# Kernel tuning notes

Measured on AMD Instinct MI355X. Metric: run time of the kernel, lower is better.

Reference implementation:

```python
import jax, jax.numpy as jnp
import numpy as np

B = 32; NPG = 500; N = B * NPG; E = 256000; F = 1024; OD = 128
DD = 80; TD = 32; NH = 4; DH = TD // NH; DFF = 128; NL = 2
LSUB = 128; MAXLEN = 4 * LSUB
NEG = -1e9; SLOPE = 0.01; EPS = 1e-5


def setup_inputs() -> dict:
    key = jax.random.key(0)
    ks = iter(jax.random.split(key, 64))
    nrm = lambda *s: jax.random.normal(next(ks), s, jnp.float32)
    w = lambda *s: nrm(*s) * 0.02
    inp = {}
    inp["pro1_x"] = nrm(N, F)
    inp["pro2_x"] = nrm(N, F)
    inp["pro1_edge_index"] = jax.random.randint(next(ks), (2, E), 0, N)
    inp["pro2_edge_index"] = jax.random.randint(next(ks), (2, E), 0, N)
    inp["pro1_batch"] = jnp.repeat(jnp.arange(B), NPG)
    inp["pro2_batch"] = jnp.repeat(jnp.arange(B), NPG)
    for nm in ("mas1_straight", "mas1_flipped", "mas2_straight", "mas2_flipped"):
        inp[nm] = nrm(B, LSUB, DD)
        inp[nm + "_lengths"] = jax.random.randint(next(ks), (B,), 1, LSUB + 1)
    inp["gcn1_w"] = w(F, F); inp["gcn1_b"] = jnp.zeros(F)
    inp["gcn2_w"] = w(F, F); inp["gcn2_b"] = jnp.zeros(F)
    inp["fc1_w"] = w(OD, F); inp["fc1_b"] = jnp.zeros(OD)
    inp["fc2_w"] = w(OD, F); inp["fc2_b"] = jnp.zeros(OD)
    inp["red_w"] = w(TD - 2, DD); inp["red_b"] = jnp.zeros(TD - 2)
    inp["attn_in_w"] = w(NL, 3 * TD, TD); inp["attn_in_b"] = jnp.zeros((NL, 3 * TD))
    inp["attn_out_w"] = w(NL, TD, TD); inp["attn_out_b"] = jnp.zeros((NL, TD))
    inp["ln1_w"] = jnp.ones((NL, TD)); inp["ln1_b"] = jnp.zeros((NL, TD))
    inp["ln2_w"] = jnp.ones((NL, TD)); inp["ln2_b"] = jnp.zeros((NL, TD))
    inp["ff1_w"] = w(NL, DFF, TD); inp["ff1_b"] = jnp.zeros((NL, DFF))
    inp["ff2_w"] = w(NL, TD, DFF); inp["ff2_b"] = jnp.zeros((NL, TD))
    inp["final_w"] = w(1, 2 * OD + TD); inp["final_b"] = jnp.zeros(1)
    return inp


def _leaky(v):
    return jnp.where(v >= 0, v, SLOPE * v)


def _gcn(x, ei, W, b):
    # GCNConv: x' = D^-1/2 (A + I) D^-1/2 (x @ W^T) + b
    sl = jnp.arange(N, dtype=ei.dtype)
    src = jnp.concatenate([ei[0], sl])
    dst = jnp.concatenate([ei[1], sl])
    deg = jax.ops.segment_sum(jnp.ones(src.shape[0], x.dtype), dst, N)
    dinv = jax.lax.rsqrt(deg)
    norm = (dinv[src] * dinv[dst])[:, None]
    h = x @ W.T
    return jax.ops.segment_sum(h[src] * norm, dst, N) + b


def _gmp(x, batch):
    # global mean pool per graph
    s = jax.ops.segment_sum(x, batch, B)
    c = jax.ops.segment_sum(jnp.ones(x.shape[0], x.dtype), batch, B)
    return s / c[:, None]


def _ln(x, w, b):
    m = x.mean(-1, keepdims=True)
    v = ((x - m) ** 2).mean(-1, keepdims=True)
    return (x - m) * jax.lax.rsqrt(v + EPS) * w + b


def _forward(pro1_x, pro1_edge_index, pro1_batch, pro2_x, pro2_edge_index, pro2_batch,
             mas1_straight, mas1_flipped, mas2_straight, mas2_flipped,
             mas1_straight_lengths, mas1_flipped_lengths, mas2_straight_lengths, mas2_flipped_lengths,
             gcn1_w, gcn1_b, fc1_w, fc1_b, gcn2_w, gcn2_b, fc2_w, fc2_b,
             red_w, red_b, attn_in_w, attn_in_b, attn_out_w, attn_out_b,
             ln1_w, ln1_b, ln2_w, ln2_b, ff1_w, ff1_b, ff2_w, ff2_b,
             final_w, final_b):
    # --- graph branches (dropout = identity at inference) ---
    x1 = _leaky(_gcn(pro1_x, pro1_edge_index, gcn1_w, gcn1_b))
    x1 = _leaky(_gmp(x1, pro1_batch) @ fc1_w.T + fc1_b)           # [B, OD]
    x2 = _leaky(_gcn(pro2_x, pro2_edge_index, gcn2_w, gcn2_b))
    x2 = _leaky(_gmp(x2, pro2_batch) @ fc2_w.T + fc2_b)           # [B, OD]

    # --- vectorized ragged pack: project, append indicators, scatter to offsets ---
    inds = ((1.0, 1.0), (0.0, 1.0), (1.0, 0.0), (0.0, 0.0))      # (straight, first)
    mas = (mas1_straight, mas1_flipped, mas2_straight, mas2_flipped)
    lens = (mas1_straight_lengths, mas1_flipped_lengths, mas2_straight_lengths, mas2_flipped_lengths)
    pos = jnp.arange(LSUB)
    brow = jnp.arange(B)[:, None]
    seq = jnp.zeros((B, MAXLEN, TD), jnp.float32)
    off = jnp.zeros((B,), lens[0].dtype)
    for m, l, (si, fi) in zip(mas, lens, inds):
        proj = m @ red_w.T + red_b                                # [B, LSUB, TD-2]
        ones = jnp.ones((B, LSUB, 1), jnp.float32)
        p = jnp.concatenate([proj, si * ones, fi * ones], -1)    # [B, LSUB, TD]
        valid = pos[None, :] < l[:, None]                        # [B, LSUB]
        idx = jnp.where(valid, off[:, None] + pos[None, :], 0)
        seq = seq.at[brow, idx].add(p * valid[..., None])
        off = off + l
    mask = jnp.arange(MAXLEN)[None, :] < off[:, None]            # [B, MAXLEN] True = valid

    # --- post-norm TransformerEncoder (relu FFN, key padding mask) ---
    x_t = seq
    for li in range(NL):
        qkv = x_t @ attn_in_w[li].T + attn_in_b[li]
        q, k, v = jnp.split(qkv, 3, axis=-1)
        q = q.reshape(B, MAXLEN, NH, DH)
        k = k.reshape(B, MAXLEN, NH, DH)
        v = v.reshape(B, MAXLEN, NH, DH)
        scores = jnp.einsum('bqhd,bkhd->bhqk', q, k) / np.float32(np.sqrt(DH))
        scores = jnp.where(mask[:, None, None, :], scores, NEG)
        attn = jax.nn.softmax(scores, axis=-1)
        o = jnp.einsum('bhqk,bkhd->bqhd', attn, v).reshape(B, MAXLEN, TD)
        o = o @ attn_out_w[li].T + attn_out_b[li]
        x_t = _ln(x_t + o, ln1_w[li], ln1_b[li])
        h = jax.nn.relu(x_t @ ff1_w[li].T + ff1_b[li]) @ ff2_w[li].T + ff2_b[li]
        x_t = _ln(x_t + h, ln2_w[li], ln2_b[li])

    mf = mask[..., None].astype(jnp.float32)
    mas_out = (x_t * mf).sum(1) / mf.sum(1)                      # masked mean [B, TD]

    combined = jnp.concatenate([x1, x2, mas_out], axis=1)        # [B, 2*OD + TD]
    return combined @ final_w.T + final_b                        # [B, 1]


def reference(pro1_x, pro1_edge_index, pro1_batch, pro2_x, pro2_edge_index, pro2_batch,
              mas1_straight, mas1_flipped, mas2_straight, mas2_flipped,
              mas1_straight_lengths, mas1_flipped_lengths, mas2_straight_lengths, mas2_flipped_lengths,
              gcn1_w, gcn1_b, fc1_w, fc1_b, gcn2_w, gcn2_b, fc2_w, fc2_b,
              red_w, red_b, attn_in_w, attn_in_b, attn_out_w, attn_out_b,
              ln1_w, ln1_b, ln2_w, ln2_b, ff1_w, ff1_b, ff2_w, ff2_b,
              final_w, final_b):
    return _forward(pro1_x, pro1_edge_index, pro1_batch, pro2_x, pro2_edge_index, pro2_batch,
                    mas1_straight, mas1_flipped, mas2_straight, mas2_flipped,
                    mas1_straight_lengths, mas1_flipped_lengths, mas2_straight_lengths, mas2_flipped_lengths,
                    gcn1_w, gcn1_b, fc1_w, fc1_b, gcn2_w, gcn2_b, fc2_w, fc2_b,
                    red_w, red_b, attn_in_w, attn_in_b, attn_out_w, attn_out_b,
                    ln1_w, ln1_b, ln2_w, ln2_b, ff1_w, ff1_b, ff2_w, ff2_b,
                    final_w, final_b)
```

## Files before the change

### kernel.cpp

```cpp
#include <hip/hip_runtime.h>
#include <stdint.h>

#define N_NODES 16000
#define MPAD_   16128
#define B_      32
#define NPG_    500
#define E_      256000
#define F_      1024
#define OD_     128
#define DD_     80
#define TD_     32
#define NH_     4
#define DH_     8
#define DFF_    128
#define LSUB_   128
#define MAXLEN_ 512
#define EPS_    1e-5f
#define SLOPE_  0.01f

typedef __bf16 bf16x8 __attribute__((ext_vector_type(8)));
typedef float  f32x4  __attribute__((ext_vector_type(4)));
typedef unsigned u32x4 __attribute__((ext_vector_type(4)));

__device__ __forceinline__ float leaky(float v) { return v >= 0.f ? v : SLOPE_ * v; }

__device__ __forceinline__ unsigned short f2bf(float f) {
  unsigned u = __float_as_uint(f);
  u += 0x7FFFu + ((u >> 16) & 1u);
  return (unsigned short)(u >> 16);
}
__device__ __forceinline__ float bf2f(unsigned short u) {
  return __uint_as_float((unsigned)u << 16);
}
__device__ __forceinline__ float bflo(unsigned u) { return __uint_as_float(u << 16); }
__device__ __forceinline__ float bfhi(unsigned u) { return __uint_as_float(u & 0xffff0000u); }
__device__ __forceinline__ unsigned pk2bf(float lo, float hi) {
  return (unsigned)f2bf(lo) | ((unsigned)f2bf(hi) << 16);
}

__device__ __forceinline__ void gld_lds16(const void* g, void* l) {
  __builtin_amdgcn_global_load_lds(
      (const __attribute__((address_space(1))) unsigned int*)g,
      (__attribute__((address_space(3))) unsigned int*)l, 16, 0, 0);
}

__global__ void k_prep(const float* __restrict__ x0, const float* __restrict__ x1,
                       const float* __restrict__ w0, const float* __restrict__ w1,
                       unsigned short* __restrict__ xb0, unsigned short* __restrict__ xb1,
                       unsigned short* __restrict__ wb0, unsigned short* __restrict__ wb1,
                       int* __restrict__ cnt) {
  const int y = blockIdx.y;
  int i = blockIdx.x * 256 + threadIdx.x;
  const int stride = gridDim.x * 256;
  if (y == 4) {
    int4 z = make_int4(0, 0, 0, 0);
    for (; i < (2 * N_NODES) / 4; i += stride) ((int4*)cnt)[i] = z;
    return;
  }
  const float* in = (y == 0) ? x0 : (y == 1) ? x1 : (y == 2) ? w0 : w1;
  unsigned short* out = (y == 0) ? xb0 : (y == 1) ? xb1 : (y == 2) ? wb0 : wb1;
  const int n4 = (y < 2) ? (N_NODES * F_ / 4) : (F_ * F_ / 4);
  for (; i < n4; i += stride) {
    float4 v = ((const float4*)in)[i];
    ushort4 o;
    o.x = f2bf(v.x); o.y = f2bf(v.y); o.z = f2bf(v.z); o.w = f2bf(v.w);
    ((ushort4*)out)[i] = o;
  }
}

#define LDSA(bf, ks, row) (*(const bf16x8*)&lds[(bf)*16384 + (ks)*8192 + (row)*32 + rs])
#define LDSB(bf, ks, row) (*(const bf16x8*)&lds[32768 + (bf)*16384 + (ks)*8192 + (row)*32 + rs])
#define STG_A(bf, R, kti) do { \
  gld_lds16(&Ag[(size_t)(mBase + (R) + r4) * 1024 + (kti) * 64 + c4],      &lds[(bf)*16384 + (R)*32 + t*8]); \
  gld_lds16(&Ag[(size_t)(mBase + (R) + r4) * 1024 + (kti) * 64 + 32 + c4], &lds[(bf)*16384 + 8192 + (R)*32 + t*8]); \
} while (0)
#define STG_B(bf, R, kti) do { \
  gld_lds16(&Bg[(size_t)(nBase + (R) + r4) * 1024 + (kti) * 64 + c4],      &lds[32768 + (bf)*16384 + (R)*32 + t*8]); \
  gld_lds16(&Bg[(size_t)(nBase + (R) + r4) * 1024 + (kti) * 64 + 32 + c4], &lds[32768 + (bf)*16384 + 8192 + (R)*32 + t*8]); \
} while (0)
#define RD_Q0(bf) do { \
  _Pragma("unroll") for (int mi = 0; mi < 4; ++mi) \
  _Pragma("unroll") for (int ks = 0; ks < 2; ++ks) \
    aLo[mi][ks] = LDSA(bf, ks, wrow * 128 + mi * 16 + l15); \
  _Pragma("unroll") for (int ni = 0; ni < 2; ++ni) \
  _Pragma("unroll") for (int ks = 0; ks < 2; ++ks) \
    bLo[ni][ks] = LDSB(bf, ks, wcol * 64 + ni * 16 + l15); \
} while (0)
#define RD_BHI(bf) do { \
  _Pragma("unroll") for (int ni = 0; ni < 2; ++ni) \
  _Pragma("unroll") for (int ks = 0; ks < 2; ++ks) \
    bHi[ni][ks] = LDSB(bf, ks, wcol * 64 + (2 + ni) * 16 + l15); \
} while (0)
#define RD_AHI(bf) do { \
  _Pragma("unroll") for (int mi = 0; mi < 4; ++mi) \
  _Pragma("unroll") for (int ks = 0; ks < 2; ++ks) \
    aHi[mi][ks] = LDSA(bf, ks, wrow * 128 + (4 + mi) * 16 + l15); \
} while (0)
#define MM_Q0() do { __builtin_amdgcn_s_setprio(1); \
  _Pragma("unroll") for (int mi = 0; mi < 4; ++mi) \
  _Pragma("unroll") for (int ni = 0; ni < 2; ++ni) \
  _Pragma("unroll") for (int ks = 0; ks < 2; ++ks) \
    acc[mi][ni] = __builtin_amdgcn_mfma_f32_16x16x32_bf16(aLo[mi][ks], bLo[ni][ks], acc[mi][ni], 0, 0, 0); \
  __builtin_amdgcn_s_setprio(0); } while (0)
#define MM_Q1() do { __builtin_amdgcn_s_setprio(1); \
  _Pragma("unroll") for (int mi = 0; mi < 4; ++mi) \
  _Pragma("unroll") for (int ni = 0; ni < 2; ++ni) \
  _Pragma("unroll") for (int ks = 0; ks < 2; ++ks) \
    acc[mi][2 + ni] = __builtin_amdgcn_mfma_f32_16x16x32_bf16(aLo[mi][ks], bHi[ni][ks], acc[mi][2 + ni], 0, 0, 0); \
  __builtin_amdgcn_s_setprio(0); } while (0)
#define MM_Q3() do { __builtin_amdgcn_s_setprio(1); \
  _Pragma("unroll") for (int mi = 0; mi < 4; ++mi) \
  _Pragma("unroll") for (int ni = 0; ni < 2; ++ni) \
  _Pragma("unroll") for (int ks = 0; ks < 2; ++ks) \
    acc[4 + mi][2 + ni] = __builtin_amdgcn_mfma_f32_16x16x32_bf16(aHi[mi][ks], bHi[ni][ks], acc[4 + mi][2 + ni], 0, 0, 0); \
  __builtin_amdgcn_s_setprio(0); } while (0)
#define MM_Q2() do { __builtin_amdgcn_s_setprio(1); \
  _Pragma("unroll") for (int mi = 0; mi < 4; ++mi) \
  _Pragma("unroll") for (int ni = 0; ni < 2; ++ni) \
  _Pragma("unroll") for (int ks = 0; ks < 2; ++ks) \
    acc[4 + mi][ni] = __builtin_amdgcn_mfma_f32_16x16x32_bf16(aHi[mi][ks], bLo[ni][ks], acc[4 + mi][ni], 0, 0, 0); \
  __builtin_amdgcn_s_setprio(0); } while (0)
#define BAR() do { __builtin_amdgcn_sched_barrier(0); __builtin_amdgcn_s_barrier(); \
                   __builtin_amdgcn_sched_barrier(0); } while (0)
#define LGKM0() do { asm volatile("s_waitcnt lgkmcnt(0)" ::: "memory"); \
                     __builtin_amdgcn_sched_barrier(0); } while (0)
#define VM4() do { asm volatile("s_waitcnt vmcnt(4)" ::: "memory"); } while (0)
#define VM0() do { asm volatile("s_waitcnt vmcnt(0)" ::: "memory"); } while (0)

__global__ __launch_bounds__(512, 2) void k_gemm256(const unsigned short* __restrict__ Ag,
                                                    const unsigned short* __restrict__ Bg,
                                                    unsigned short* __restrict__ Cg) {
  __shared__ short lds[65536];
  const int j  = blockIdx.x;
  const int x8 = j & 7;
  const int chunk = (x8 < 4) ? x8 * 32 : 128 + (x8 - 4) * 31;
  const int pos = chunk + (j >> 3);
  const int mb = pos >> 2, nb = pos & 3;
  const size_t g = blockIdx.z;
  Ag += g * (size_t)MPAD_ * 1024;
  Bg += g * (size_t)1024 * 1024;
  Cg += g * (size_t)MPAD_ * 1024;
  const int t = threadIdx.x;
  const int lane = t & 63, wave = t >> 6;
  const int wrow = wave >> 2, wcol = wave & 3;
  const int quad = lane >> 4, l15 = lane & 15;
  const int mBase = mb * 256, nBase = nb * 256;
  const int r4 = t >> 2;
  const int c4 = (((t & 3) - ((t >> 3) & 3)) & 3) * 8;
  const int rs = ((quad + (l15 >> 1)) & 3) * 8;

  f32x4 acc[8][4];
  f32x4 zero = {0.f, 0.f, 0.f, 0.f};
#pragma unroll
  for (int i = 0; i < 8; ++i)
#pragma unroll
    for (int jn = 0; jn < 4; ++jn) acc[i][jn] = zero;

  bf16x8 aLo[4][2], aHi[4][2], bLo[2][2], bHi[2][2];

  STG_A(0, 0, 0); STG_A(0, 128, 0); STG_B(0, 0, 0); STG_B(0, 128, 0);
  STG_B(1, 0, 1); STG_B(1, 128, 1);
  VM4();
  BAR();

  for (int kt = 0; kt < 16; kt += 2) {
    const bool s2 = (kt + 2) < 16;
    const bool s3 = (kt + 3) < 16;
    RD_Q0(0);
    STG_A(1, 0, kt + 1);
    BAR(); LGKM0(); MM_Q0(); BAR();
    RD_BHI(0);
    STG_A(1, 128, kt + 1);
    BAR(); LGKM0(); MM_Q1(); BAR();
    RD_AHI(0);
    if (s2) STG_B(0, 0, kt + 2);
    BAR(); LGKM0(); MM_Q3(); BAR();
    if (s2) { STG_B(0, 128, kt + 2); VM4(); } else VM0();
    BAR(); MM_Q2(); BAR();
    RD_Q0(1);
    if (s2) STG_A(0, 0, kt + 2);
    BAR(); LGKM0(); MM_Q0(); BAR();
    RD_BHI(1);
    if (s2) STG_A(0, 128, kt + 2);
    BAR(); LGKM0(); MM_Q1(); BAR();
    RD_AHI(1);
    if (s3) STG_B(1, 0, kt + 3);
    BAR(); LGKM0(); MM_Q3(); BAR();
    if (s3) { STG_B(1, 128, kt + 3); VM4(); }
    BAR(); MM_Q2(); BAR();
  }

#pragma unroll
  for (int mi = 0; mi < 8; ++mi)
#pragma unroll
    for (int ni = 0; ni < 4; ++ni)
#pragma unroll
      for (int r = 0; r < 4; ++r) {
        int grow = mBase + wrow * 128 + mi * 16 + quad * 4 + r;
        int gcol = nBase + wcol * 64 + ni * 16 + l15;
        Cg[(size_t)grow * 1024 + gcol] = f2bf(acc[mi][ni][r]);
      }
}

__global__ void k_hist(const int* __restrict__ ei0, const int* __restrict__ ei1,
                       int* __restrict__ cnt, int e, int n) {
  const int g = blockIdx.y;
  const int* dst = (g ? ei1 : ei0) + e;
  int i = blockIdx.x * 256 + threadIdx.x;
  if (i < e) atomicAdd(&cnt[g * n + dst[i]], 1);
}

__global__ void k_scan(const int* __restrict__ cnt_all, int* __restrict__ rowstart_all,
                       int* __restrict__ cursor_all, float* __restrict__ dinv_all, int n) {
  const int g = blockIdx.x;
  const int* cnt = cnt_all + g * n;
  int* rowstart = rowstart_all + g * (n + 1);
  int* cursor   = cursor_all + g * n;
  float* dinv   = dinv_all + g * n;
  __shared__ int part[256];
  __shared__ int base[257];
  int t = threadIdx.x;
  int chunk = (n + 255) >> 8;
  int s = 0;
  for (int j = 0; j < chunk; ++j) {
    int idx = t * chunk + j;
    if (idx < n) s += cnt[idx];
  }
  part[t] = s;
  __syncthreads();
  if (t == 0) {
    int a = 0;
    for (int i = 0; i < 256; ++i) { base[i] = a; a += part[i]; }
    base[256] = a;
  }
  __syncthreads();
  int a = base[t];
  for (int j = 0; j < chunk; ++j) {
    int idx = t * chunk + j;
    if (idx < n) {
      int c = cnt[idx];
      rowstart[idx] = a; cursor[idx] = a; a += c;
      dinv[idx] = rsqrtf((float)c + 1.0f);
    }
  }
  if (t == 0) rowstart[n] = base[256];
}

__global__ void k_scatter(const int* __restrict__ ei0, const int* __restrict__ ei1,
                          const float* __restrict__ dinv_all, int* __restrict__ cursor_all,
                          int2* __restrict__ csre_all, int e, int n) {
  const int g = blockIdx.y;
  const int* ei = g ? ei1 : ei0;
  int i = blockIdx.x * 256 + threadIdx.x;
  if (i < e) {
    int s = ei[i], d = ei[e + i];
    int p = atomicAdd(&cursor_all[g * n + d], 1);
    float w = dinv_all[g * n + s] * dinv_all[g * n + d];
    csre_all[(size_t)g * e + p] = make_int2(s, __float_as_int(w));
  }
}

__global__ __launch_bounds__(256) void k_gather(const uint4* __restrict__ h8_all,
                                                const float* __restrict__ dinv_all,
                                                const int* __restrict__ rowstart_all,
                                                const int2* __restrict__ csre_all,
                                                unsigned* __restrict__ aggs_all) {
  const int g = blockIdx.z;
  const uint4* h8 = h8_all + (size_t)g * MPAD_ * 128;
  const float* dinv = dinv_all + (size_t)g * N_NODES;
  const int* rowstart = rowstart_all + (size_t)g * (N_NODES + 1);
  const int2* csre = csre_all + (size_t)g * E_;
  const int sl = blockIdx.x;
  const int t = threadIdx.x;
  const int wv = t >> 6, lane = t & 63;
  const int qtr = lane >> 4, l16 = lane & 15;
  const int i = blockIdx.y * 16 + wv * 4 + qtr;
  const int fo8 = sl * 16 + l16;
  const float di = dinv[i];
  const float selfw = di * di;
  uint4 sv = h8[(size_t)i * 128 + fo8];
  float a0 = bflo(sv.x) * selfw, a1 = bfhi(sv.x) * selfw;
  float a2 = bflo(sv.y) * selfw, a3 = bfhi(sv.y) * selfw;
  float a4 = bflo(sv.z) * selfw, a5 = bfhi(sv.z) * selfw;
  float a6 = bflo(sv.w) * selfw, a7 = bfhi(sv.w) * selfw;
  int j = rowstart[i];
  const int end = rowstart[i + 1];
  for (; j + 2 <= end; j += 2) {
    int2 e0 = csre[j], e1 = csre[j + 1];
    uint4 v0 = h8[(size_t)e0.x * 128 + fo8];
    uint4 v1 = h8[(size_t)e1.x * 128 + fo8];
    float w0 = __int_as_float(e0.y), w1 = __int_as_float(e1.y);
    a0 += bflo(v0.x) * w0 + bflo(v1.x) * w1;
    a1 += bfhi(v0.x) * w0 + bfhi(v1.x) * w1;
    a2 += bflo(v0.y) * w0 + bflo(v1.y) * w1;
    a3 += bfhi(v0.y) * w0 + bfhi(v1.y) * w1;
    a4 += bflo(v0.z) * w0 + bflo(v1.z) * w1;
    a5 += bfhi(v0.z) * w0 + bfhi(v1.z) * w1;
    a6 += bflo(v0.w) * w0 + bflo(v1.w) * w1;
    a7 += bfhi(v0.w) * w0 + bfhi(v1.w) * w1;
  }
  if (j < end) {
    int2 e0 = csre[j];
    uint4 v0 = h8[(size_t)e0.x * 128 + fo8];
    float w0 = __int_as_float(e0.y);
    a0 += bflo(v0.x) * w0; a1 += bfhi(v0.x) * w0;
    a2 += bflo(v0.y) * w0; a3 += bfhi(v0.y) * w0;
    a4 += bflo(v0.z) * w0; a5 += bfhi(v0.z) * w0;
    a6 += bflo(v0.w) * w0; a7 += bfhi(v0.w) * w0;
  }
  u32x4 o;
  o.x = pk2bf(a0, a1); o.y = pk2bf(a2, a3);
  o.z = pk2bf(a4, a5); o.w = pk2bf(a6, a7);
  u32x4* dst = (u32x4*)&aggs_all[(((size_t)(g * 8 + sl) * N_NODES + i) * 16 + l16) * 4];
  __builtin_nontemporal_store(o, dst);
}

__global__ __launch_bounds__(512) void k_poolpart(const unsigned short* __restrict__ aggs,
                                                  const float* __restrict__ bias0,
                                                  const float* __restrict__ bias1,
                                                  float* __restrict__ partial) {
  const int b = blockIdx.x, g = blockIdx.y, c = blockIdx.z;
  const int t = threadIdx.x;
  const int sl = t >> 6, o = t & 63;
  const float* bias = g ? bias1 : bias0;
  const float bf0 = bias[t * 2], bf1 = bias[t * 2 + 1];
  const ushort2* base = (const ushort2*)aggs + ((size_t)(g * 8 + sl) * N_NODES) * 64 + o;
  const int r0 = b * NPG_ + c * 100;
  float s0 = 0.f, s1 = 0.f;
  for (int r = 0; r < 100; ++r) {
    ushort2 v = base[(size_t)(r0 + r) * 64];
    s0 += leaky(bf2f(v.x) + bf0);
    s1 += leaky(bf2f(v.y) + bf1);
  }
  *(float2*)&partial[(((size_t)c * 2 + g) * B_ + b) * F_ + t * 2] = make_float2(s0, s1);
}

__global__ __launch_bounds__(256) void k_fc(const float* __restrict__ partial,
                     const float* __restrict__ w0, const float* __restrict__ w1,
                     const float* __restrict__ bias0, const float* __restrict__ bias1,
                     float* __restrict__ out0, float* __restrict__ out1) {
  __shared__ float ps[F_];
  const int b = blockIdx.x, g = blockIdx.y, t = threadIdx.x;
  const float* w = g ? w1 : w0;
  const float* bias = g ? bias1 : bias0;
  float* out = g ? out1 : out0;
  float4 s = {0.f, 0.f, 0.f, 0.f};
#pragma unroll
  for (int c = 0; c < 5; ++c) {
    float4 v = ((const float4*)(partial + (((size_t)c * 2 + g) * B_ + b) * F_))[t];
    s.x += v.x; s.y += v.y; s.z += v.z; s.w += v.w;
  }
  ((float4*)ps)[t] = s;
  __syncthreads();
  const int wave = t >> 6, lane = t & 63;
  for (int oo = 0; oo < 32; ++oo) {
    const int o = wave * 32 + oo;
    const float* wr = w + (size_t)o * F_;
    float a = 0.f;
#pragma unroll
    for (int c = 0; c < 16; ++c) a += wr[c * 64 + lane] * ps[c * 64 + lane];
#pragma unroll
    for (int m = 1; m < 64; m <<= 1) a += __shfl_xor(a, m, 64);
    if (lane == 0) out[b * OD_ + o] = leaky(a * (1.f / 500.f) + bias[o]);
  }
}

__global__ void k_pack(const float* __restrict__ m0, const float* __restrict__ m1,
                       const float* __restrict__ m2, const float* __restrict__ m3,
                       const int* __restrict__ l0, const int* __restrict__ l1,
                       const int* __restrict__ l2, const int* __restrict__ l3,
                       const float* __restrict__ rw, const float* __restrict__ rb,
                       float* __restrict__ seq, int* __restrict__ tot) {
  __shared__ float xs[DD_];
  const int p = blockIdx.x, b = blockIdx.y, k = blockIdx.z;
  const float* mas = (k == 0) ? m0 : (k == 1) ? m1 : (k == 2) ? m2 : m3;
  const int*   lk  = (k == 0) ? l0 : (k == 1) ? l1 : (k == 2) ? l2 : l3;
  const int len = lk[b];
  if (p >= len) return;
  int off = 0;
  if (k > 0) off += l0[b];
  if (k > 1) off += l1[b];
  if (k > 2) off += l2[b];
  const int t = threadIdx.x;
  if (p == 0 && k == 0 && t == 63) tot[b] = l0[b] + l1[b] + l2[b] + l3[b];
  for (int d = t; d < DD_; d += 64) xs[d] = mas[(size_t)(b * LSUB_ + p) * DD_ + d];
  __syncthreads();
  if (t < TD_) {
    float v;
    if (t < TD_ - 2) {
      float a = rb[t];
      const float* w = &rw[t * DD_];
      for (int d = 0; d < DD_; ++d) a += xs[d] * w[d];
      v = a;
    } else if (t == TD_ - 2) {
      v = (k == 0 || k == 2) ? 1.f : 0.f;
    } else {
      v = (k < 2) ? 1.f : 0.f;
    }
    seq[((size_t)b * MAXLEN_ + off + p) * TD_ + t] = v;
  }
}

__global__ __launch_bounds__(512) void k_qkv(const float* __restrict__ xt,
                                             const float* __restrict__ w,
                                             const float* __restrict__ bias,
                                             const int* __restrict__ tot,
                                             float* __restrict__ Qp,
                                             float* __restrict__ Kp,
                                             float* __restrict__ Vp) {
  __shared__ float xs[4][TD_];
  const int u = threadIdx.x >> 7;
  const int t = threadIdx.x & 127;
  const int row = blockIdx.x * 4 + u;
  const int b = row >> 9, p = row & (MAXLEN_ - 1);
  const bool alive = p < tot[b];
  if (alive && t < TD_) xs[u][t] = xt[(size_t)row * TD_ + t];
  __syncthreads();
  if (!alive || t >= 3 * TD_) return;
  float a = bias[t];
  const float* wr = &w[t * TD_];
#pragma unroll
  for (int k = 0; k < TD_; ++k) a += xs[u][k] * wr[k];
  if (t < 32) {
    Qp[(size_t)row * 32 + t] = a;
  } else if (t < 64) {
    int h = (t - 32) >> 3, d = (t - 32) & 7;
    Kp[(((size_t)b * NH_ + h) * MAXLEN_ + p) * DH_ + d] = a;
  } else {
    int h = (t - 64) >> 3, d = (t - 64) & 7;
    Vp[(((size_t)b * NH_ + h) * MAXLEN_ + p) * DH_ + d] = a;
  }
}

__global__ __launch_bounds__(128) void k_attn(const float* __restrict__ Qp,
                                              const float* __restrict__ Kp,
                                              const float* __restrict__ Vp,
                                              const int* __restrict__ tot,
                                              float* __restrict__ obuf) {
  __shared__ float Kl[MAXLEN_ * DH_];
  __shared__ float Vl[MAXLEN_ * DH_];
  const int h = blockIdx.x, b = blockIdx.y, qz = blockIdx.z;
  const int t = threadIdx.x;
  const int L = tot[b];
  if (qz * 64 >= L) return;
  const float* Kpl = Kp + ((size_t)b * NH_ + h) * MAXLEN_ * DH_;
  const float* Vpl = Vp + ((size_t)b * NH_ + h) * MAXLEN_ * DH_;
  const int n4 = (L * DH_ + 3) >> 2;
  for (int i = t; i < n4; i += 128) {
    ((float4*)Kl)[i] = ((const float4*)Kpl)[i];
    ((float4*)Vl)[i] = ((const float4*)Vpl)[i];
  }
  __syncthreads();
  const int qi = qz * 64 + (t >> 1);
  if (qi >= L) return;
  const int half = t & 1;
  const float scale = 0.35355339059327373f;
  float q[8];
#pragma unroll
  for (int d = 0; d < 8; ++d) q[d] = Qp[((size_t)b * MAXLEN_ + qi) * TD_ + h * 8 + d] * scale;

  float l0 = 0.f, l1 = 0.f;
  float a0[8] = {0, 0, 0, 0, 0, 0, 0, 0};
  float a1[8] = {0, 0, 0, 0, 0, 0, 0, 0};
  int j = half;
  for (; j + 2 < L; j += 4) {
    const float* kr0 = &Kl[j * 8];
    const float* kr1 = &Kl[(j + 2) * 8];
    float s0 = 0.f, s1 = 0.f;
#pragma unroll
    for (int d = 0; d < 8; ++d) { s0 += q[d] * kr0[d]; s1 += q[d] * kr1[d]; }
    float p0 = __expf(s0), p1 = __expf(s1);
    l0 += p0; l1 += p1;
    const float* vr0 = &Vl[j * 8];
    const float* vr1 = &Vl[(j + 2) * 8];
#pragma unroll
    for (int d = 0; d < 8; ++d) { a0[d] += p0 * vr0[d]; a1[d] += p1 * vr1[d]; }
  }
  for (; j < L; j += 2) {
    const float* kr = &Kl[j * 8];
    float s = 0.f;
#pragma unroll
    for (int d = 0; d < 8; ++d) s += q[d] * kr[d];
    float p = __expf(s);
    l0 += p;
    const float* vr = &Vl[j * 8];
#pragma unroll
    for (int d = 0; d < 8; ++d) a0[d] += p * vr[d];
  }
  float l = l0 + l1;
#pragma unroll
  for (int d = 0; d < 8; ++d) a0[d] += a1[d];
  l += __shfl_xor(l, 1);
#pragma unroll
  for (int d = 0; d < 8; ++d) a0[d] += __shfl_xor(a0[d], 1);
  float inv = 1.f / l;
  const int dbase = half * 4;
  float4 o;
  o.x = a0[dbase + 0] * inv; o.y = a0[dbase + 1] * inv;
  o.z = a0[dbase + 2] * inv; o.w = a0[dbase + 3] * inv;
  *(float4*)&obuf[((size_t)b * MAXLEN_ + qi) * TD_ + h * 8 + dbase] = o;
}

__global__ __launch_bounds__(128) void k_post(const float* __restrict__ obuf,
                                              const float* __restrict__ ow,
                                              const float* __restrict__ ob,
                                              const float* __restrict__ l1w,
                                              const float* __restrict__ l1b,
                                              const float* __restrict__ f1w,
                                              const float* __restrict__ f1b,
                                              const float* __restrict__ f2w,
                                              const float* __restrict__ f2b,
                                              const float* __restrict__ l2w,
                                              const float* __restrict__ l2b,
                                              const int* __restrict__ tot,
                                              float* __restrict__ xt) {
  const int r = blockIdx.x, t = threadIdx.x;
  if ((r & (MAXLEN_ - 1)) >= tot[r >> 9]) return;
  __shared__ float xs[TD_];
  __shared__ float hb[DFF_];
  if (t < TD_) {
    const float* orow = &obuf[(size_t)r * TD_];
    float a = ob[t] + xt[(size_t)r * TD_ + t];
    const float* wr = &ow[t * TD_];
#pragma unroll
    for (int k = 0; k < TD_; ++k) a += orow[k] * wr[k];
    float s1 = a, s2 = a * a;
#pragma unroll
    for (int m = 1; m < 32; m <<= 1) {
      s1 += __shfl_xor(s1, m, 32);
      s2 += __shfl_xor(s2, m, 32);
    }
    float mean = s1 * (1.f / 32.f);
    float var  = s2 * (1.f / 32.f) - mean * mean;
    xs[t] = (a - mean) * rsqrtf(var + EPS_) * l1w[t] + l1b[t];
  }
  __syncthreads();
  {
    float a = f1b[t];
    const float* wr = &f1w[t * TD_];
#pragma unroll
    for (int k = 0; k < TD_; ++k) a += xs[k] * wr[k];
    hb[t] = fmaxf(a, 0.f);
  }
  __syncthreads();
  if (t < TD_) {
    float a = f2b[t] + xs[t];
    const float* wr = &f2w[t * DFF_];
#pragma unroll
    for (int k = 0; k < DFF_; ++k) a += hb[k] * wr[k];
    float s1 = a, s2 = a * a;
#pragma unroll
    for (int m = 1; m < 32; m <<= 1) {
      s1 += __shfl_xor(s1, m, 32);
      s2 += __shfl_xor(s2, m, 32);
    }
    float mean = s1 * (1.f / 32.f);
    float var  = s2 * (1.f / 32.f) - mean * mean;
    xt[(size_t)r * TD_ + t] = (a - mean) * rsqrtf(var + EPS_) * l2w[t] + l2b[t];
  }
}

__global__ __launch_bounds__(256) void k_maskfinal(const float* __restrict__ xt,
                                                   const int* __restrict__ tot,
                                                   const float* __restrict__ x1,
                                                   const float* __restrict__ x2,
                                                   const float* __restrict__ fw,
                                                   const float* __restrict__ fb,
                                                   float* __restrict__ out) {
  __shared__ float sbuf[8][32];
  __shared__ float mo[TD_];
  const int b = blockIdx.x, t = threadIdx.x;
  const int j = t & 31, c = t >> 5;
  const int L = tot[b];
  float s = 0.f;
  for (int p = c; p < L; p += 8) s += xt[((size_t)b * MAXLEN_ + p) * TD_ + j];
  sbuf[c][j] = s;
  __syncthreads();
  if (t < 32) {
    float a = 0.f;
#pragma unroll
    for (int cc = 0; cc < 8; ++cc) a += sbuf[cc][t];
    mo[t] = a / (float)L;
  }
  __syncthreads();
  if (t < 64) {
    float s2 = 0.f;
    for (int i = t; i < 2 * OD_ + TD_; i += 64) {
      float cv = (i < OD_) ? x1[b * OD_ + i]
               : (i < 2 * OD_) ? x2[b * OD_ + (i - OD_)]
               : mo[i - 2 * OD_];
      s2 += fw[i] * cv;
    }
#pragma unroll
    for (int m = 1; m < 64; m <<= 1) s2 += __shfl_xor(s2, m, 64);
    if (t == 0) out[b] = s2 + fb[0];
  }
}

extern "C" void kernel_launch(void* const* d_in, const int* in_sizes, int n_in,
                              void* d_out, int out_size, void* d_ws, size_t ws_size,
                              hipStream_t stream) {
  (void)in_sizes; (void)n_in; (void)out_size; (void)ws_size;
  const float* pro_x[2]  = {(const float*)d_in[0], (const float*)d_in[1]};
  const int*   pro_ei[2] = {(const int*)d_in[2], (const int*)d_in[3]};
  const float* mas[4]    = {(const float*)d_in[6], (const float*)d_in[8],
                            (const float*)d_in[10], (const float*)d_in[12]};
  const int*   lens[4]   = {(const int*)d_in[7], (const int*)d_in[9],
                            (const int*)d_in[11], (const int*)d_in[13]};
  const float* gw[2]  = {(const float*)d_in[14], (const float*)d_in[16]};
  const float* gb[2]  = {(const float*)d_in[15], (const float*)d_in[17]};
  const float* fcw[2] = {(const float*)d_in[18], (const float*)d_in[20]};
  const float* fcb[2] = {(const float*)d_in[19], (const float*)d_in[21]};
  const float* red_w = (const float*)d_in[22];
  const float* red_b = (const float*)d_in[23];
  const float* attn_in_w  = (const float*)d_in[24];
  const float* attn_in_b  = (const float*)d_in[25];
  const float* attn_out_w = (const float*)d_in[26];
  const float* attn_out_b = (const float*)d_in[27];
  const float* ln1_w = (const float*)d_in[28];
  const float* ln1_b = (const float*)d_in[29];
  const float* ln2_w = (const float*)d_in[30];
  const float* ln2_b = (const float*)d_in[31];
  const float* ff1_w = (const float*)d_in[32];
  const float* ff1_b = (const float*)d_in[33];
  const float* ff2_w = (const float*)d_in[34];
  const float* ff2_b = (const float*)d_in[35];
  const float* final_w = (const float*)d_in[36];
  const float* final_b = (const float*)d_in[37];
  float* out = (float*)d_out;

  char* p = (char*)d_ws;
  auto carve = [&](size_t bytes) -> void* {
    void* r = (void*)p;
    p += (bytes + 255) & ~(size_t)255;
    return r;
  };
  unsigned short* xb  = (unsigned short*)carve((size_t)2 * MPAD_ * F_ * 2);
  unsigned short* Wb  = (unsigned short*)carve((size_t)2 * F_ * F_ * 2);
  unsigned short* h   = (unsigned short*)carve((size_t)2 * MPAD_ * F_ * 2);
  unsigned short* aggs = (unsigned short*)carve((size_t)2 * 8 * N_NODES * 128 * 2);
  int*   cnt      = (int*)carve((size_t)2 * N_NODES * 4);
  float* dinv     = (float*)carve((size_t)2 * N_NODES * 4);
  int*   rowstart = (int*)carve((size_t)2 * (N_NODES + 1) * 4);
  int*   cursor   = (int*)carve((size_t)2 * N_NODES * 4);
  int2*  csre     = (int2*)carve((size_t)2 * E_ * 8);
  float* partial  = (float*)carve((size_t)5 * 2 * B_ * F_ * 4);
  float* xg[2];
  xg[0] = (float*)carve((size_t)B_ * OD_ * 4);
  xg[1] = (float*)carve((size_t)B_ * OD_ * 4);
  float* seq    = (float*)carve((size_t)B_ * MAXLEN_ * TD_ * 4);
  float* Qp     = (float*)carve((size_t)B_ * MAXLEN_ * TD_ * 4);
  float* Kp     = (float*)carve((size_t)B_ * NH_ * MAXLEN_ * DH_ * 4);
  float* Vp     = (float*)carve((size_t)B_ * NH_ * MAXLEN_ * DH_ * 4);
  float* obuf   = (float*)carve((size_t)B_ * MAXLEN_ * TD_ * 4);
  int*   totlen = (int*)carve((size_t)B_ * 4);

  k_prep<<<dim3(1024, 5), 256, 0, stream>>>(pro_x[0], pro_x[1], gw[0], gw[1],
                                            xb, xb + (size_t)MPAD_ * F_,
                                            Wb, Wb + (size_t)F_ * F_, cnt);
  k_gemm256<<<dim3(252, 1, 2), 512, 0, stream>>>(xb, Wb, h);
  k_hist<<<dim3(1000, 2), 256, 0, stream>>>(pro_ei[0], pro_ei[1], cnt, E_, N_NODES);
  k_scan<<<2, 256, 0, stream>>>(cnt, rowstart, cursor, dinv, N_NODES);
  k_scatter<<<dim3(1000, 2), 256, 0, stream>>>(pro_ei[0], pro_ei[1], dinv, cursor,
                                               csre, E_, N_NODES);
  k_gather<<<dim3(8, 1000, 2), 256, 0, stream>>>((const uint4*)h, dinv, rowstart,
                                                 csre, (unsigned*)aggs);
  k_poolpart<<<dim3(B_, 2, 5), 512, 0, stream>>>(aggs, gb[0], gb[1], partial);
  k_fc<<<dim3(B_, 2), 256, 0, stream>>>(partial, fcw[0], fcw[1], fcb[0], fcb[1],
                                        xg[0], xg[1]);

  k_pack<<<dim3(LSUB_, B_, 4), 64, 0, stream>>>(mas[0], mas[1], mas[2], mas[3],
                                                lens[0], lens[1], lens[2], lens[3],
                                                red_w, red_b, seq, totlen);

  for (int li = 0; li < 2; ++li) {
    k_qkv<<<(B_ * MAXLEN_) / 4, 512, 0, stream>>>(seq, attn_in_w + (size_t)li * 96 * TD_,
                                                  attn_in_b + (size_t)li * 96, totlen,
                                                  Qp, Kp, Vp);
    k_attn<<<dim3(NH_, B_, 8), 128, 0, stream>>>(Qp, Kp, Vp, totlen, obuf);
    k_post<<<B_ * MAXLEN_, 128, 0, stream>>>(
        obuf, attn_out_w + (size_t)li * TD_ * TD_, attn_out_b + (size_t)li * TD_,
        ln1_w + (size_t)li * TD_, ln1_b + (size_t)li * TD_,
        ff1_w + (size_t)li * DFF_ * TD_, ff1_b + (size_t)li * DFF_,
        ff2_w + (size_t)li * TD_ * DFF_, ff2_b + (size_t)li * TD_,
        ln2_w + (size_t)li * TD_, ln2_b + (size_t)li * TD_, totlen, seq);
  }

  k_maskfinal<<<B_, 256, 0, stream>>>(seq, totlen, xg[0], xg[1], final_w, final_b, out);
}
```

Before: 721.2 us.

## Fuse bias+leaky+mean-pool into gather; process four rows per post block

The gather kernel now applies bias and leaky ReLU and reduces node rows per graph through shared memory and atomicAdd into a pooled buffer. This removes the bf16 aggregate write, the separate poolpart kernel and the partial-sum reduction in k_fc. The pooled buffer is zeroed in k_prep. Separately, k_post handles four sequence rows per 128-thread block instead of one, so fewer blocks are launched and more of each block's lanes do work. In exchange, the fused pooling uses float atomics, making summation order nondeterministic, and adds two block syncs per gather block.

```diff
diff --git a/kernel.cpp b/kernel.cpp
--- a/kernel.cpp
+++ b/kernel.cpp
@@ -20,7 +20,6 @@
 
 typedef __bf16 bf16x8 __attribute__((ext_vector_type(8)));
 typedef float  f32x4  __attribute__((ext_vector_type(4)));
-typedef unsigned u32x4 __attribute__((ext_vector_type(4)));
 
 __device__ __forceinline__ float leaky(float v) { return v >= 0.f ? v : SLOPE_ * v; }
 
@@ -34,9 +33,6 @@
 }
 __device__ __forceinline__ float bflo(unsigned u) { return __uint_as_float(u << 16); }
 __device__ __forceinline__ float bfhi(unsigned u) { return __uint_as_float(u & 0xffff0000u); }
-__device__ __forceinline__ unsigned pk2bf(float lo, float hi) {
-  return (unsigned)f2bf(lo) | ((unsigned)f2bf(hi) << 16);
-}
 
 __device__ __forceinline__ void gld_lds16(const void* g, void* l) {
   __builtin_amdgcn_global_load_lds(
@@ -48,13 +44,15 @@
                        const float* __restrict__ w0, const float* __restrict__ w1,
                        unsigned short* __restrict__ xb0, unsigned short* __restrict__ xb1,
                        unsigned short* __restrict__ wb0, unsigned short* __restrict__ wb1,
-                       int* __restrict__ cnt) {
+                       int* __restrict__ cnt, float* __restrict__ pooled) {
   const int y = blockIdx.y;
   int i = blockIdx.x * 256 + threadIdx.x;
   const int stride = gridDim.x * 256;
   if (y == 4) {
     int4 z = make_int4(0, 0, 0, 0);
-    for (; i < (2 * N_NODES) / 4; i += stride) ((int4*)cnt)[i] = z;
+    for (int idx = i; idx < (2 * N_NODES) / 4; idx += stride) ((int4*)cnt)[idx] = z;
+    float4 zf = {0.f, 0.f, 0.f, 0.f};
+    for (int idx = i; idx < (2 * B_ * F_) / 4; idx += stride) ((float4*)pooled)[idx] = zf;
     return;
   }
   const float* in = (y == 0) ? x0 : (y == 1) ? x1 : (y == 2) ? w0 : w1;
@@ -264,7 +262,9 @@
                                                 const float* __restrict__ dinv_all,
                                                 const int* __restrict__ rowstart_all,
                                                 const int2* __restrict__ csre_all,
-                                                unsigned* __restrict__ aggs_all) {
+                                                const float* __restrict__ bias0,
+                                                const float* __restrict__ bias1,
+                                                float* __restrict__ pooled) {
   const int g = blockIdx.z;
   const uint4* h8 = h8_all + (size_t)g * MPAD_ * 128;
   const float* dinv = dinv_all + (size_t)g * N_NODES;
@@ -308,49 +308,53 @@
     a4 += bflo(v0.z) * w0; a5 += bfhi(v0.z) * w0;
     a6 += bflo(v0.w) * w0; a7 += bfhi(v0.w) * w0;
   }
-  u32x4 o;
-  o.x = pk2bf(a0, a1); o.y = pk2bf(a2, a3);
-  o.z = pk2bf(a4, a5); o.w = pk2bf(a6, a7);
-  u32x4* dst = (u32x4*)&aggs_all[(((size_t)(g * 8 + sl) * N_NODES + i) * 16 + l16) * 4];
-  __builtin_nontemporal_store(o, dst);
-}
-
-__global__ __launch_bounds__(512) void k_poolpart(const unsigned short* __restrict__ aggs,
-                                                  const float* __restrict__ bias0,
-                                                  const float* __restrict__ bias1,
-                                                  float* __restrict__ partial) {
-  const int b = blockIdx.x, g = blockIdx.y, c = blockIdx.z;
-  const int t = threadIdx.x;
-  const int sl = t >> 6, o = t & 63;
-  const float* bias = g ? bias1 : bias0;
-  const float bf0 = bias[t * 2], bf1 = bias[t * 2 + 1];
-  const ushort2* base = (const ushort2*)aggs + ((size_t)(g * 8 + sl) * N_NODES) * 64 + o;
-  const int r0 = b * NPG_ + c * 100;
-  float s0 = 0.f, s1 = 0.f;
-  for (int r = 0; r < 100; ++r) {
-    ushort2 v = base[(size_t)(r0 + r) * 64];
-    s0 += leaky(bf2f(v.x) + bf0);
-    s1 += leaky(bf2f(v.y) + bf1);
-  }
-  *(float2*)&partial[(((size_t)c * 2 + g) * B_ + b) * F_ + t * 2] = make_float2(s0, s1);
-}
-
-__global__ __launch_bounds__(256) void k_fc(const float* __restrict__ partial,
+  const float* gbias = g ? bias1 : bias0;
+  const int f0 = fo8 * 8;
+  float pk[8];
+  pk[0] = leaky(a0 + gbias[f0 + 0]); pk[1] = leaky(a1 + gbias[f0 + 1]);
+  pk[2] = leaky(a2 + gbias[f0 + 2]); pk[3] = leaky(a3 + gbias[f0 + 3]);
+  pk[4] = leaky(a4 + gbias[f0 + 4]); pk[5] = leaky(a5 + gbias[f0 + 5]);
+  pk[6] = leaky(a6 + gbias[f0 + 6]); pk[7] = leaky(a7 + gbias[f0 + 7]);
+  __shared__ float sacc[4][16][8];
+  const int i0 = blockIdx.y * 16;
+  const int b0 = i0 / NPG_, b1 = (i0 + 15) / NPG_;
+  const int myb = i / NPG_;
+  const int npass = (b0 == b1) ? 1 : 2;
+  for (int pass = 0; pass < npass; ++pass) {
+    const int bt = pass ? b1 : b0;
+    float v[8];
+#pragma unroll
+    for (int k = 0; k < 8; ++k) {
+      float x = (myb == bt) ? pk[k] : 0.f;
+      x += __shfl_xor(x, 16);
+      x += __shfl_xor(x, 32);
+      v[k] = x;
+    }
+    if (qtr == 0) {
+#pragma unroll
+      for (int k = 0; k < 8; ++k) sacc[wv][l16][k] = v[k];
+    }
+    __syncthreads();
+    if (t < 128) {
+      const int li = t >> 3, kk = t & 7;
+      float tot = sacc[0][li][kk] + sacc[1][li][kk] + sacc[2][li][kk] + sacc[3][li][kk];
+      atomicAdd(&pooled[(((size_t)g * B_ + bt) << 10) + sl * 128 + t], tot);
+    }
+    __syncthreads();
+  }
+}
+
+__global__ __launch_bounds__(256) void k_fc(const float* __restrict__ pooled,
                      const float* __restrict__ w0, const float* __restrict__ w1,
                      const float* __restrict__ bias0, const float* __restrict__ bias1,
                      float* __restrict__ out0, float* __restrict__ out1) {
   __shared__ float ps[F_];
   const int b = blockIdx.x, g = blockIdx.y, t = threadIdx.x;
+  const float* p = pooled + ((size_t)g * B_ + b) * F_;
   const float* w = g ? w1 : w0;
   const float* bias = g ? bias1 : bias0;
   float* out = g ? out1 : out0;
-  float4 s = {0.f, 0.f, 0.f, 0.f};
-#pragma unroll
-  for (int c = 0; c < 5; ++c) {
-    float4 v = ((const float4*)(partial + (((size_t)c * 2 + g) * B_ + b) * F_))[t];
-    s.x += v.x; s.y += v.y; s.z += v.z; s.w += v.w;
-  }
-  ((float4*)ps)[t] = s;
+  ((float4*)ps)[t] = ((const float4*)p)[t];
   __syncthreads();
   const int wave = t >> 6, lane = t & 63;
   for (int oo = 0; oo < 32; ++oo) {
@@ -514,14 +518,20 @@
                                               const float* __restrict__ l2b,
                                               const int* __restrict__ tot,
                                               float* __restrict__ xt) {
-  const int r = blockIdx.x, t = threadIdx.x;
-  if ((r & (MAXLEN_ - 1)) >= tot[r >> 9]) return;
-  __shared__ float xs[TD_];
-  __shared__ float hb[DFF_];
-  if (t < TD_) {
+  const int t = threadIdx.x;
+  const int r0 = blockIdx.x * 4;
+  const int b = r0 >> 9;
+  const int L = tot[b];
+  if ((r0 & (MAXLEN_ - 1)) >= L) return;
+  const int u = t >> 5, jj = t & 31;
+  const int r = r0 + u;
+  const bool alive = (r & (MAXLEN_ - 1)) < L;
+  __shared__ float xs[4][TD_];
+  __shared__ float hb[4][DFF_];
+  if (alive) {
     const float* orow = &obuf[(size_t)r * TD_];
-    float a = ob[t] + xt[(size_t)r * TD_ + t];
-    const float* wr = &ow[t * TD_];
+    float a = ob[jj] + xt[(size_t)r * TD_ + jj];
+    const float* wr = &ow[jj * TD_];
 #pragma unroll
     for (int k = 0; k < TD_; ++k) a += orow[k] * wr[k];
     float s1 = a, s2 = a * a;
@@ -532,22 +542,25 @@
     }
     float mean = s1 * (1.f / 32.f);
     float var  = s2 * (1.f / 32.f) - mean * mean;
-    xs[t] = (a - mean) * rsqrtf(var + EPS_) * l1w[t] + l1b[t];
-  }
-  __syncthreads();
-  {
-    float a = f1b[t];
-    const float* wr = &f1w[t * TD_];
-#pragma unroll
-    for (int k = 0; k < TD_; ++k) a += xs[k] * wr[k];
-    hb[t] = fmaxf(a, 0.f);
-  }
-  __syncthreads();
-  if (t < TD_) {
-    float a = f2b[t] + xs[t];
-    const float* wr = &f2w[t * DFF_];
-#pragma unroll
-    for (int k = 0; k < DFF_; ++k) a += hb[k] * wr[k];
+    xs[u][jj] = (a - mean) * rsqrtf(var + EPS_) * l1w[jj] + l1b[jj];
+  }
+  __syncthreads();
+#pragma unroll
+  for (int it = 0; it < 4; ++it) {
+    if ((((r0 + it) & (MAXLEN_ - 1)) < L)) {
+      float a = f1b[t];
+      const float* wr = &f1w[t * TD_];
+#pragma unroll
+      for (int k = 0; k < TD_; ++k) a += xs[it][k] * wr[k];
+      hb[it][t] = fmaxf(a, 0.f);
+    }
+  }
+  __syncthreads();
+  if (alive) {
+    float a = f2b[jj] + xs[u][jj];
+    const float* wr = &f2w[jj * DFF_];
+#pragma unroll
+    for (int k = 0; k < DFF_; ++k) a += hb[u][k] * wr[k];
     float s1 = a, s2 = a * a;
 #pragma unroll
     for (int m = 1; m < 32; m <<= 1) {
@@ -556,7 +569,7 @@
     }
     float mean = s1 * (1.f / 32.f);
     float var  = s2 * (1.f / 32.f) - mean * mean;
-    xt[(size_t)r * TD_ + t] = (a - mean) * rsqrtf(var + EPS_) * l2w[t] + l2b[t];
+    xt[(size_t)r * TD_ + jj] = (a - mean) * rsqrtf(var + EPS_) * l2w[jj] + l2b[jj];
   }
 }
 
@@ -638,13 +651,12 @@
   unsigned short* xb  = (unsigned short*)carve((size_t)2 * MPAD_ * F_ * 2);
   unsigned short* Wb  = (unsigned short*)carve((size_t)2 * F_ * F_ * 2);
   unsigned short* h   = (unsigned short*)carve((size_t)2 * MPAD_ * F_ * 2);
-  unsigned short* aggs = (unsigned short*)carve((size_t)2 * 8 * N_NODES * 128 * 2);
   int*   cnt      = (int*)carve((size_t)2 * N_NODES * 4);
   float* dinv     = (float*)carve((size_t)2 * N_NODES * 4);
   int*   rowstart = (int*)carve((size_t)2 * (N_NODES + 1) * 4);
   int*   cursor   = (int*)carve((size_t)2 * N_NODES * 4);
   int2*  csre     = (int2*)carve((size_t)2 * E_ * 8);
-  float* partial  = (float*)carve((size_t)5 * 2 * B_ * F_ * 4);
+  float* pooled   = (float*)carve((size_t)2 * B_ * F_ * 4);
   float* xg[2];
   xg[0] = (float*)carve((size_t)B_ * OD_ * 4);
   xg[1] = (float*)carve((size_t)B_ * OD_ * 4);
@@ -657,16 +669,15 @@
 
   k_prep<<<dim3(1024, 5), 256, 0, stream>>>(pro_x[0], pro_x[1], gw[0], gw[1],
                                             xb, xb + (size_t)MPAD_ * F_,
-                                            Wb, Wb + (size_t)F_ * F_, cnt);
+                                            Wb, Wb + (size_t)F_ * F_, cnt, pooled);
   k_gemm256<<<dim3(252, 1, 2), 512, 0, stream>>>(xb, Wb, h);
   k_hist<<<dim3(1000, 2), 256, 0, stream>>>(pro_ei[0], pro_ei[1], cnt, E_, N_NODES);
   k_scan<<<2, 256, 0, stream>>>(cnt, rowstart, cursor, dinv, N_NODES);
   k_scatter<<<dim3(1000, 2), 256, 0, stream>>>(pro_ei[0], pro_ei[1], dinv, cursor,
                                                csre, E_, N_NODES);
   k_gather<<<dim3(8, 1000, 2), 256, 0, stream>>>((const uint4*)h, dinv, rowstart,
-                                                 csre, (unsigned*)aggs);
-  k_poolpart<<<dim3(B_, 2, 5), 512, 0, stream>>>(aggs, gb[0], gb[1], partial);
-  k_fc<<<dim3(B_, 2), 256, 0, stream>>>(partial, fcw[0], fcw[1], fcb[0], fcb[1],
+                                                 csre, gb[0], gb[1], pooled);
+  k_fc<<<dim3(B_, 2), 256, 0, stream>>>(pooled, fcw[0], fcw[1], fcb[0], fcb[1],
                                         xg[0], xg[1]);
 
   k_pack<<<dim3(LSUB_, B_, 4), 64, 0, stream>>>(mas[0], mas[1], mas[2], mas[3],
@@ -678,7 +689,7 @@
                                                   attn_in_b + (size_t)li * 96, totlen,
                                                   Qp, Kp, Vp);
     k_attn<<<dim3(NH_, B_, 8), 128, 0, stream>>>(Qp, Kp, Vp, totlen, obuf);
-    k_post<<<B_ * MAXLEN_, 128, 0, stream>>>(
+    k_post<<<(B_ * MAXLEN_) / 4, 128, 0, stream>>>(
         obuf, attn_out_w + (size_t)li * TD_ * TD_, attn_out_b + (size_t)li * TD_,
         ln1_w + (size_t)li * TD_, ln1_b + (size_t)li * TD_,
         ff1_w + (size_t)li * DFF_ * TD_, ff1_b + (size_t)li * DFF_,
```

New measurement: 734.6 us. About the same (+1.9%).
